# Performance work log

Hardware: AMD Instinct MI355X
Metric: run time of the kernel (lower is better)

Reference implementation:

```python
import jax, jax.numpy as jnp
import numpy as np

B, S, D, H, DK, FF, NQ = 4, 1024, 512, 64, 8, 2048, 8


def _layernorm(x, w, b, eps=1e-5):
    m = x.mean(-1, keepdims=True)
    v = ((x - m) ** 2).mean(-1, keepdims=True)
    return (x - m) / jnp.sqrt(v + eps) * w + b


def setup_inputs() -> dict:
    key = jax.random.key(0)
    ks = jax.random.split(key, 24)
    std = 0.02
    inp = {
        "x": jax.random.normal(ks[0], (B, S, D), dtype=jnp.float32),
        "Wq": jax.random.normal(ks[1], (D, D)) * std,
        "bq": jnp.zeros((D,)),
        "Wk": jax.random.normal(ks[2], (D, D)) * std,
        "bk": jnp.zeros((D,)),
        "Wv": jax.random.normal(ks[3], (D, D)) * std,
        "bv": jnp.zeros((D,)),
        "theta_attn": jax.random.normal(ks[4], (DK,)) * 0.1,  # trainable RX angles
        "gate_attn": jnp.asarray(1.0, dtype=jnp.float32),
        "Wo": jax.random.normal(ks[5], (D, D)) * std,
        "bo": jnp.zeros((D,)),
        "ln1_w": jnp.ones((D,)),
        "ln1_b": jnp.zeros((D,)),
        "W1": jax.random.normal(ks[6], (FF, NQ)) * std,
        "b1": jnp.zeros((FF,)),
        "W2": jax.random.normal(ks[7], (D, FF)) * std,
        "b2": jnp.zeros((D,)),
        "phi_ffn": jax.random.normal(ks[8], (NQ,)) * 0.1,  # trainable RY angles
        "gate_ffn": jnp.asarray(1.0, dtype=jnp.float32),
        "ln2_w": jnp.ones((D,)),
        "ln2_b": jnp.zeros((D,)),
    }
    return inp


def _attention(x, Wq, bq, Wk, bk, Wv, bv, theta, gate, Wo, bo):
    q = x @ Wq.T + bq
    k = x @ Wk.T + bk
    v = x @ Wv.T + bv
    sep = lambda t: t.reshape(B, S, H, DK).transpose(0, 2, 1, 3)  # [B,H,S,DK]
    qh, kh, vh = sep(q), sep(k), sep(v)
    scores = jnp.einsum("bhsd,bhtd->bhst", qh, kh) / np.sqrt(DK)
    probs = jax.nn.softmax(scores, axis=-1)
    classical = jnp.einsum("bhst,bhtd->bhsd", probs, vh)
    classical = classical.transpose(0, 2, 1, 3).reshape(B, S, D)
    # Quantum head: RX(x_i) then RX(theta_i) -> RX(x_i+theta_i), CNOT ring, <Z_j>.
    # Analytic expectations: <Z_0> = prod_{k=1..DK-1} cos(a_k);
    #                        <Z_j> = prod_{k=0..j}    cos(a_k)   (j >= 1).
    cos_a = jnp.cos(qh + theta)  # [B,H,S,DK]
    cp = jnp.cumprod(cos_a, axis=-1)
    z0 = jnp.prod(cos_a[..., 1:], axis=-1, keepdims=True)
    quantum = jnp.concatenate([z0, cp[..., 1:]], axis=-1)  # [B,H,S,DK]
    quantum = quantum.transpose(0, 2, 1, 3).reshape(B, S, D)
    out = gate * quantum + (1.0 - gate) * classical
    return out @ Wo.T + bo


def _ffn(x, W1, b1, W2, b2, phi, gate):
    xs = x[..., :NQ]  # encoder uses first NQ features
    # Quantum: RX(x_i) then RY(phi_i), measure <Z_i> = cos(x_i)*cos(phi_i).
    qm = jnp.cos(xs) * jnp.cos(phi)
    quantum = jax.nn.relu(qm @ W1.T + b1) @ W2.T + b2
    classical = jax.nn.relu(xs @ W1.T + b1) @ W2.T + b2
    return gate * quantum + (1.0 - gate) * classical


def reference(x, Wq, bq, Wk, bk, Wv, bv, theta_attn, gate_attn, Wo, bo,
              ln1_w, ln1_b, W1, b1, W2, b2, phi_ffn, gate_ffn, ln2_w, ln2_b):
    attn_out = _attention(x, Wq, bq, Wk, bk, Wv, bv, theta_attn, gate_attn, Wo, bo)
    x1 = _layernorm(x + attn_out, ln1_w, ln1_b)
    ffn_out = _ffn(x1, W1, b1, W2, b2, phi_ffn, gate_ffn)
    return _layernorm(x1 + ffn_out, ln2_w, ln2_b)
```

## Files before the change

### kernel.cpp

```cpp
#include <hip/hip_runtime.h>
#include <hip/hip_bf16.h>


typedef short short8 __attribute__((ext_vector_type(8)));
typedef float floatx4 __attribute__((ext_vector_type(4)));

__device__ __forceinline__ unsigned short f2bf_bits(float f) {
  __hip_bfloat16 h = __float2bfloat16(f);
  return *reinterpret_cast<unsigned short*>(&h);
}
__device__ __forceinline__ float bfbits2f(unsigned short u) {
  union { unsigned int u; float f; } c;
  c.u = (unsigned int)u << 16;
  return c.f;
}

#define GLOBAL_LOAD_LDS16(g, l)                                               \
  __builtin_amdgcn_global_load_lds(                                           \
      (const __attribute__((address_space(1))) void*)(g),                     \
      (__attribute__((address_space(3))) void*)(l), 16, 0, 0)

#define WAIT_VMCNT0()   asm volatile("s_waitcnt vmcnt(0)" ::: "memory")
#define WAIT_VMCNT16()  asm volatile("s_waitcnt vmcnt(16)" ::: "memory")
#define WAIT_LGKM0()    asm volatile("s_waitcnt lgkmcnt(0)" ::: "memory")

__device__ __forceinline__ void gemm_core(
    const __hip_bfloat16* __restrict__ A,
    const __hip_bfloat16* __restrict__ W,
    int K, long m0, long n0, int lane,
    __hip_bfloat16* sh, floatx4 acc[4][4])
{
  const int srow = lane >> 3;
  const int schunk = lane & 7;
  const int gchunk = schunk ^ srow;
  const int frow = lane & 15;
  const int fk = lane >> 4;

  auto stage = [&](int kt, __hip_bfloat16* Ab, __hip_bfloat16* Bb) {
#pragma unroll
    for (int ib = 0; ib < 8; ++ib) {
      const int row = ib * 8 + srow;
      GLOBAL_LOAD_LDS16(A + (m0 + row) * K + kt + gchunk * 8, Ab + ib * 512);
      GLOBAL_LOAD_LDS16(W + (n0 + row) * K + kt + gchunk * 8, Bb + ib * 512);
    }
  };

  const int ntiles = K >> 6;
  stage(0, sh, sh + 4096);
  for (int t = 0; t < ntiles; ++t) {
    __hip_bfloat16* As = sh + (t & 1) * 8192;
    __hip_bfloat16* Bs = As + 4096;
    if (t + 1 < ntiles) {
      WAIT_LGKM0();
      __hip_bfloat16* An = sh + ((t + 1) & 1) * 8192;
      stage((t + 1) << 6, An, An + 4096);
      WAIT_VMCNT16();
    } else {
      WAIT_VMCNT0();
    }
    short8 af[2][4], bf[2][4];
#pragma unroll
    for (int ks = 0; ks < 2; ++ks)
#pragma unroll
      for (int i = 0; i < 4; ++i) {
        const int ar = i * 16 + frow;
        af[ks][i] = *(const short8*)(As + ar * 64 + (((ks * 4 + fk) ^ (ar & 7)) << 3));
        bf[ks][i] = *(const short8*)(Bs + ar * 64 + (((ks * 4 + fk) ^ (ar & 7)) << 3));
      }
#pragma unroll
    for (int ks = 0; ks < 2; ++ks)
#pragma unroll
      for (int i = 0; i < 4; ++i)
#pragma unroll
        for (int j = 0; j < 4; ++j)
          acc[i][j] = __builtin_amdgcn_mfma_f32_16x16x32_bf16(
              af[ks][i], bf[ks][j], acc[i][j], 0, 0, 0);
  }
}

__global__ __launch_bounds__(64) void gemm_qkv(
    const __hip_bfloat16* __restrict__ x_bf,
    const __hip_bfloat16* __restrict__ Wq,
    const __hip_bfloat16* __restrict__ Wk,
    const __hip_bfloat16* __restrict__ Wv,
    const float* __restrict__ bq, const float* __restrict__ bk,
    const float* __restrict__ bvv,
    __hip_bfloat16* __restrict__ mix,
    float* __restrict__ Qb, float* __restrict__ Kb, float* __restrict__ Vb,
    const float* __restrict__ theta, const float* __restrict__ gateA)
{
  const int z = blockIdx.z;
  const float g = *gateA;
  if (z > 0 && g == 1.0f) return;
  const __hip_bfloat16* W = (z == 0) ? Wq : (z == 1) ? Wk : Wv;
  const float* bias = (z == 0) ? bq : (z == 1) ? bk : bvv;
  float* Cf = (z == 0) ? Qb : (z == 1) ? Kb : Vb;

  __shared__ __align__(16) __hip_bfloat16 sh[16384];
  const int lane = threadIdx.x;
  const long m0 = (long)blockIdx.x * 64;
  const long n0 = (long)blockIdx.y * 64;
  floatx4 acc[4][4];
#pragma unroll
  for (int i = 0; i < 4; ++i)
#pragma unroll
    for (int j = 0; j < 4; ++j) acc[i][j] = (floatx4){0.f, 0.f, 0.f, 0.f};

  gemm_core(x_bf, W, 512, m0, n0, lane, sh, acc);

  const int col_l = lane & 15;
  const int row_l = (lane >> 4) << 2;

  if (z > 0 || g != 1.0f) {
#pragma unroll
    for (int j = 0; j < 4; ++j) {
      const long col = n0 + j * 16 + col_l;
      const float bv = bias[col];
#pragma unroll
      for (int i = 0; i < 4; ++i)
#pragma unroll
        for (int r = 0; r < 4; ++r)
          Cf[(m0 + i * 16 + row_l + r) * 512 + col] = acc[i][j][r] + bv;
    }
  }
  if (z == 0) {
    float* shf = (float*)sh;
    WAIT_LGKM0();
#pragma unroll
    for (int j = 0; j < 4; ++j) {
      const long col = n0 + j * 16 + col_l;
      const float bv = bias[col];
#pragma unroll
      for (int i = 0; i < 4; ++i)
#pragma unroll
        for (int r = 0; r < 4; ++r)
          shf[(i * 16 + row_l + r) * 64 + j * 16 + col_l] = acc[i][j][r] + bv;
    }
    WAIT_LGKM0();
    float th[8];
#pragma unroll
    for (int i = 0; i < 8; ++i) th[i] = theta[i];
#pragma unroll
    for (int t = 0; t < 8; ++t) {
      const int gidx = t * 64 + lane;
      const int row = gidx >> 3;
      const int hh = gidx & 7;
      const float* src = shf + row * 64 + hh * 8;
      float c[8];
#pragma unroll
      for (int i = 0; i < 8; ++i) c[i] = __cosf(src[i] + th[i]);
      float o[8];
      float p = c[1];
#pragma unroll
      for (int i = 2; i < 8; ++i) p *= c[i];
      o[0] = p;
      float cp = c[0];
#pragma unroll
      for (int i = 1; i < 8; ++i) { cp *= c[i]; o[i] = cp; }
      union { unsigned short u16[8]; uint4 v; } pk;
#pragma unroll
      for (int i = 0; i < 8; ++i) pk.u16[i] = f2bf_bits(o[i]);
      *(uint4*)(mix + (m0 + row) * 512 + n0 + hh * 8) = pk.v;
    }
  }
}

__global__ __launch_bounds__(64) void gemm_plain(
    const __hip_bfloat16* __restrict__ A,
    const __hip_bfloat16* __restrict__ W,
    const float* __restrict__ bias, float* __restrict__ C, int N, int K)
{
  __shared__ __align__(16) __hip_bfloat16 sh[16384];
  const int lane = threadIdx.x;
  const long m0 = (long)blockIdx.x * 64;
  const long n0 = (long)blockIdx.y * 64;
  floatx4 acc[4][4];
#pragma unroll
  for (int i = 0; i < 4; ++i)
#pragma unroll
    for (int j = 0; j < 4; ++j) acc[i][j] = (floatx4){0.f, 0.f, 0.f, 0.f};
  gemm_core(A, W, K, m0, n0, lane, sh, acc);
  const int col_l = lane & 15;
  const int row_l = (lane >> 4) << 2;
#pragma unroll
  for (int j = 0; j < 4; ++j) {
    const long col = n0 + j * 16 + col_l;
    const float bv = bias[col];
#pragma unroll
    for (int i = 0; i < 4; ++i)
#pragma unroll
      for (int r = 0; r < 4; ++r)
        C[(m0 + i * 16 + row_l + r) * N + col] = acc[i][j][r] + bv;
  }
}

__global__ __launch_bounds__(64) void gemm_ffnout(
    const __hip_bfloat16* __restrict__ hq,
    const __hip_bfloat16* __restrict__ hc,
    const __hip_bfloat16* __restrict__ W2, const float* __restrict__ b2,
    float* __restrict__ Fb, float* __restrict__ Fc,
    const float* __restrict__ gateF)
{
  const int z = blockIdx.z;
  if (z == 1 && *gateF == 1.0f) return;
  const __hip_bfloat16* A = z ? hc : hq;
  float* C = z ? Fc : Fb;
  __shared__ __align__(16) __hip_bfloat16 sh[16384];
  const int lane = threadIdx.x;
  const long m0 = (long)blockIdx.x * 64;
  const long n0 = (long)blockIdx.y * 64;
  floatx4 acc[4][4];
#pragma unroll
  for (int i = 0; i < 4; ++i)
#pragma unroll
    for (int j = 0; j < 4; ++j) acc[i][j] = (floatx4){0.f, 0.f, 0.f, 0.f};
  gemm_core(A, W2, 2048, m0, n0, lane, sh, acc);
  const int col_l = lane & 15;
  const int row_l = (lane >> 4) << 2;
#pragma unroll
  for (int j = 0; j < 4; ++j) {
    const long col = n0 + j * 16 + col_l;
    const float bv = b2[col];
#pragma unroll
    for (int i = 0; i < 4; ++i)
#pragma unroll
      for (int r = 0; r < 4; ++r)
        C[(m0 + i * 16 + row_l + r) * 512 + col] = acc[i][j][r] + bv;
  }
}

__device__ __forceinline__ void cvt_one(const float* s, __hip_bfloat16* d, int n,
                                        long tid, long stride) {
  const int n4 = n >> 2;
  for (long i = tid; i < n4; i += stride) {
    float4 v = ((const float4*)s)[i];
    ushort4 u;
    u.x = f2bf_bits(v.x); u.y = f2bf_bits(v.y);
    u.z = f2bf_bits(v.z); u.w = f2bf_bits(v.w);
    ((ushort4*)d)[i] = u;
  }
}

__global__ __launch_bounds__(256) void prep_inputs(
    const float* x, __hip_bfloat16* x_bf,
    const float* Wq, __hip_bfloat16* Wq_bf,
    const float* Wo, __hip_bfloat16* Wo_bf,
    const float* W2, __hip_bfloat16* W2_bf,
    const float* W1, __hip_bfloat16* W1_bf,
    const float* Wk, __hip_bfloat16* Wk_bf,
    const float* Wv, __hip_bfloat16* Wv_bf,
    const float* gateA)
{
  const long stride = (long)gridDim.x * blockDim.x;
  const long tid = (long)blockIdx.x * blockDim.x + threadIdx.x;
  cvt_one(x, x_bf, 4096 * 512, tid, stride);
  cvt_one(Wq, Wq_bf, 512 * 512, tid, stride);
  cvt_one(Wo, Wo_bf, 512 * 512, tid, stride);
  cvt_one(W2, W2_bf, 512 * 2048, tid, stride);
  cvt_one(W1, W1_bf, 2048 * 8, tid, stride);
  if (*gateA != 1.0f) {
    cvt_one(Wk, Wk_bf, 512 * 512, tid, stride);
    cvt_one(Wv, Wv_bf, 512 * 512, tid, stride);
  }
}

__global__ __launch_bounds__(256) void attn_blend(
    const float* __restrict__ Qb, const float* __restrict__ Kb,
    const float* __restrict__ Vb, __hip_bfloat16* __restrict__ mix,
    const float* __restrict__ gateA)
{
  const float g = *gateA;
  if (g == 1.0f) return;
  const int idx = blockIdx.x * blockDim.x + threadIdx.x;
  if (idx >= 4 * 64 * 1024) return;
  const int s = idx & 1023;
  const int h = (idx >> 10) & 63;
  const int b = idx >> 16;
  const long qoff = ((long)(b * 1024 + s)) * 512 + h * 8;
  float q[8];
#pragma unroll
  for (int i = 0; i < 8; ++i) q[i] = Qb[qoff + i] * 0.35355339059327373f;
  float m = -INFINITY, l = 0.0f, acc[8];
#pragma unroll
  for (int i = 0; i < 8; ++i) acc[i] = 0.0f;
  for (int t = 0; t < 1024; ++t) {
    const long koff = ((long)(b * 1024 + t)) * 512 + h * 8;
    const float* kr = Kb + koff;
    const float* vr = Vb + koff;
    float sc = 0.0f;
#pragma unroll
    for (int i = 0; i < 8; ++i) sc += q[i] * kr[i];
    float nm = fmaxf(m, sc);
    float corr = __expf(m - nm);
    float p = __expf(sc - nm);
    l = l * corr + p;
#pragma unroll
    for (int i = 0; i < 8; ++i) acc[i] = acc[i] * corr + p * vr[i];
    m = nm;
  }
  const float inv = 1.0f / l;
  union { unsigned short u16[8]; uint4 v; } pk;
  pk.v = *(const uint4*)(mix + qoff);
#pragma unroll
  for (int i = 0; i < 8; ++i) {
    float quant = bfbits2f(pk.u16[i]);
    pk.u16[i] = f2bf_bits(g * quant + (1.0f - g) * acc[i] * inv);
  }
  *(uint4*)(mix + qoff) = pk.v;
}

__global__ __launch_bounds__(256) void lnffn2(
    const float* __restrict__ x, const float* __restrict__ attn,
    const float* __restrict__ lw, const float* __restrict__ lb,
    float* __restrict__ x1, const float* __restrict__ phi,
    const __hip_bfloat16* __restrict__ W1_bf, const float* __restrict__ b1,
    __hip_bfloat16* __restrict__ hq, __hip_bfloat16* __restrict__ hc,
    const float* __restrict__ gateF)
{
  const int tid = threadIdx.x;
  const int wv = tid >> 6, lane = tid & 63;
  const int row = blockIdx.x * 4 + wv;
  const long base = (long)row * 512;
  const int c0 = lane * 8;
  __shared__ float qrow[4][8];
  __shared__ float xsrow[4][8];

  float4 a0 = *(const float4*)(x + base + c0);
  float4 a1 = *(const float4*)(x + base + c0 + 4);
  float4 b0 = *(const float4*)(attn + base + c0);
  float4 b1v4 = *(const float4*)(attn + base + c0 + 4);
  float s[8] = {a0.x + b0.x, a0.y + b0.y, a0.z + b0.z, a0.w + b0.w,
                a1.x + b1v4.x, a1.y + b1v4.y, a1.z + b1v4.z, a1.w + b1v4.w};
  float sum = 0.f, ssq = 0.f;
#pragma unroll
  for (int i = 0; i < 8; ++i) { sum += s[i]; ssq += s[i] * s[i]; }
#pragma unroll
  for (int off = 32; off > 0; off >>= 1) {
    sum += __shfl_xor(sum, off);
    ssq += __shfl_xor(ssq, off);
  }
  const float mean = sum * (1.0f / 512.0f);
  const float var = ssq * (1.0f / 512.0f) - mean * mean;
  const float rstd = rsqrtf(fmaxf(var, 0.0f) + 1e-5f);
  float4 w0 = *(const float4*)(lw + c0);
  float4 w1 = *(const float4*)(lw + c0 + 4);
  float4 g0 = *(const float4*)(lb + c0);
  float4 g1 = *(const float4*)(lb + c0 + 4);
  float o[8];
  const float wf[8] = {w0.x, w0.y, w0.z, w0.w, w1.x, w1.y, w1.z, w1.w};
  const float gf8[8] = {g0.x, g0.y, g0.z, g0.w, g1.x, g1.y, g1.z, g1.w};
#pragma unroll
  for (int i = 0; i < 8; ++i) o[i] = (s[i] - mean) * rstd * wf[i] + gf8[i];
  *(float4*)(x1 + base + c0) = (float4){o[0], o[1], o[2], o[3]};
  *(float4*)(x1 + base + c0 + 4) = (float4){o[4], o[5], o[6], o[7]};
  if (lane == 0) {
#pragma unroll
    for (int i = 0; i < 8; ++i) {
      qrow[wv][i] = __cosf(o[i]) * __cosf(phi[i]);
      xsrow[wv][i] = o[i];
    }
  }
  __syncthreads();

  float w1f[8][8];
#pragma unroll
  for (int j = 0; j < 8; ++j) {
    uint4 wr = *(const uint4*)(W1_bf + (long)(tid * 8 + j) * 8);
    const unsigned short* pu = (const unsigned short*)&wr;
#pragma unroll
    for (int k = 0; k < 8; ++k) w1f[j][k] = bfbits2f(pu[k]);
  }
  float4 bb0 = *(const float4*)(b1 + tid * 8);
  float4 bb1 = *(const float4*)(b1 + tid * 8 + 4);
  const float b1v[8] = {bb0.x, bb0.y, bb0.z, bb0.w, bb1.x, bb1.y, bb1.z, bb1.w};
  const float gv = *gateF;
#pragma unroll
  for (int r = 0; r < 4; ++r) {
    const long rowr = (long)blockIdx.x * 4 + r;
    float qm[8];
#pragma unroll
    for (int k = 0; k < 8; ++k) qm[k] = qrow[r][k];
    union { unsigned short u16[8]; uint4 v; } pk;
#pragma unroll
    for (int j = 0; j < 8; ++j) {
      float acc = b1v[j];
#pragma unroll
      for (int k = 0; k < 8; ++k) acc += qm[k] * w1f[j][k];
      pk.u16[j] = f2bf_bits(fmaxf(acc, 0.0f));
    }
    *(uint4*)(hq + rowr * 2048 + tid * 8) = pk.v;
    if (gv != 1.0f) {
      float xs[8];
#pragma unroll
      for (int k = 0; k < 8; ++k) xs[k] = xsrow[r][k];
#pragma unroll
      for (int j = 0; j < 8; ++j) {
        float acc = b1v[j];
#pragma unroll
        for (int k = 0; k < 8; ++k) acc += xs[k] * w1f[j][k];
        pk.u16[j] = f2bf_bits(fmaxf(acc, 0.0f));
      }
      *(uint4*)(hc + rowr * 2048 + tid * 8) = pk.v;
    }
  }
}

__global__ __launch_bounds__(256) void add_ln3(
    const float* __restrict__ x1, const float* __restrict__ Fb,
    const float* __restrict__ Fc, const float* __restrict__ gateF,
    const float* __restrict__ lw, const float* __restrict__ lb,
    float* __restrict__ out)
{
  const int tid = threadIdx.x;
  const int wv = tid >> 6, lane = tid & 63;
  const int row = blockIdx.x * 4 + wv;
  const long base = (long)row * 512;
  const int c0 = lane * 8;
  float4 a0 = *(const float4*)(x1 + base + c0);
  float4 a1 = *(const float4*)(x1 + base + c0 + 4);
  float4 f0 = *(const float4*)(Fb + base + c0);
  float4 f1 = *(const float4*)(Fb + base + c0 + 4);
  float s[8];
  const float gv = *gateF;
  if (gv != 1.0f) {
    float4 c0v = *(const float4*)(Fc + base + c0);
    float4 c1v = *(const float4*)(Fc + base + c0 + 4);
    const float om = 1.0f - gv;
    s[0] = a0.x + gv * f0.x + om * c0v.x; s[1] = a0.y + gv * f0.y + om * c0v.y;
    s[2] = a0.z + gv * f0.z + om * c0v.z; s[3] = a0.w + gv * f0.w + om * c0v.w;
    s[4] = a1.x + gv * f1.x + om * c1v.x; s[5] = a1.y + gv * f1.y + om * c1v.y;
    s[6] = a1.z + gv * f1.z + om * c1v.z; s[7] = a1.w + gv * f1.w + om * c1v.w;
  } else {
    s[0] = a0.x + f0.x; s[1] = a0.y + f0.y; s[2] = a0.z + f0.z; s[3] = a0.w + f0.w;
    s[4] = a1.x + f1.x; s[5] = a1.y + f1.y; s[6] = a1.z + f1.z; s[7] = a1.w + f1.w;
  }
  float sum = 0.f, ssq = 0.f;
#pragma unroll
  for (int i = 0; i < 8; ++i) { sum += s[i]; ssq += s[i] * s[i]; }
#pragma unroll
  for (int off = 32; off > 0; off >>= 1) {
    sum += __shfl_xor(sum, off);
    ssq += __shfl_xor(ssq, off);
  }
  const float mean = sum * (1.0f / 512.0f);
  const float var = ssq * (1.0f / 512.0f) - mean * mean;
  const float rstd = rsqrtf(fmaxf(var, 0.0f) + 1e-5f);
  float4 w0 = *(const float4*)(lw + c0);
  float4 w1 = *(const float4*)(lw + c0 + 4);
  float4 g0 = *(const float4*)(lb + c0);
  float4 g1 = *(const float4*)(lb + c0 + 4);
  const float wf[8] = {w0.x, w0.y, w0.z, w0.w, w1.x, w1.y, w1.z, w1.w};
  const float gf8[8] = {g0.x, g0.y, g0.z, g0.w, g1.x, g1.y, g1.z, g1.w};
  float o[8];
#pragma unroll
  for (int i = 0; i < 8; ++i) o[i] = (s[i] - mean) * rstd * wf[i] + gf8[i];
  *(float4*)(out + base + c0) = (float4){o[0], o[1], o[2], o[3]};
  *(float4*)(out + base + c0 + 4) = (float4){o[4], o[5], o[6], o[7]};
}

extern "C" void kernel_launch(void* const* d_in, const int* in_sizes, int n_in,
                              void* d_out, int out_size, void* d_ws, size_t ws_size,
                              hipStream_t stream) {
  const float* x     = (const float*)d_in[0];
  const float* Wq    = (const float*)d_in[1];
  const float* bq    = (const float*)d_in[2];
  const float* Wk    = (const float*)d_in[3];
  const float* bk    = (const float*)d_in[4];
  const float* Wv    = (const float*)d_in[5];
  const float* bv    = (const float*)d_in[6];
  const float* theta = (const float*)d_in[7];
  const float* gateA = (const float*)d_in[8];
  const float* Wo    = (const float*)d_in[9];
  const float* bo    = (const float*)d_in[10];
  const float* ln1w  = (const float*)d_in[11];
  const float* ln1b  = (const float*)d_in[12];
  const float* W1    = (const float*)d_in[13];
  const float* b1    = (const float*)d_in[14];
  const float* W2    = (const float*)d_in[15];
  const float* b2    = (const float*)d_in[16];
  const float* phi   = (const float*)d_in[17];
  const float* gateF = (const float*)d_in[18];
  const float* ln2w  = (const float*)d_in[19];
  const float* ln2b  = (const float*)d_in[20];
  float* out = (float*)d_out;

  const size_t MB = 1024 * 1024;
  char* wsb = (char*)d_ws;
  __hip_bfloat16* x_bf   = (__hip_bfloat16*)(wsb + 0 * MB);
  __hip_bfloat16* Wq_bf  = (__hip_bfloat16*)(wsb + 4 * MB);
  __hip_bfloat16* Wo_bf  = (__hip_bfloat16*)(wsb + 4 * MB + 512 * 1024);
  __hip_bfloat16* W2_bf  = (__hip_bfloat16*)(wsb + 5 * MB);
  __hip_bfloat16* W1_bf  = (__hip_bfloat16*)(wsb + 7 * MB);
  __hip_bfloat16* mix_bf = (__hip_bfloat16*)(wsb + 8 * MB);
  float*          attn   = (float*)(wsb + 12 * MB);
  float*          x1     = (float*)(wsb + 20 * MB);
  __hip_bfloat16* hq_bf  = (__hip_bfloat16*)(wsb + 28 * MB);
  float*          Fb     = (float*)(wsb + 44 * MB);
  float*          Qb     = (float*)(wsb + 52 * MB);
  __hip_bfloat16* Wk_bf  = (__hip_bfloat16*)(wsb + 60 * MB);
  __hip_bfloat16* Wv_bf  = (__hip_bfloat16*)(wsb + 60 * MB + 512 * 1024);
  float*          Kb2    = (float*)(wsb + 61 * MB);
  float*          Vb2    = (float*)(wsb + 69 * MB);
  __hip_bfloat16* hc_bf  = (__hip_bfloat16*)(wsb + 77 * MB);
  float*          Fc     = (float*)(wsb + 93 * MB);

  prep_inputs<<<1024, 256, 0, stream>>>(
      x, x_bf, Wq, Wq_bf, Wo, Wo_bf, W2, W2_bf, W1, W1_bf,
      Wk, Wk_bf, Wv, Wv_bf, gateA);
  gemm_qkv<<<dim3(64, 8, 3), 64, 0, stream>>>(
      x_bf, Wq_bf, Wk_bf, Wv_bf, bq, bk, bv,
      mix_bf, Qb, Kb2, Vb2, theta, gateA);
  attn_blend<<<1024, 256, 0, stream>>>(Qb, Kb2, Vb2, mix_bf, gateA);
  gemm_plain<<<dim3(64, 8), 64, 0, stream>>>(
      mix_bf, Wo_bf, bo, attn, 512, 512);
  lnffn2<<<1024, 256, 0, stream>>>(
      x, attn, ln1w, ln1b, x1, phi, W1_bf, b1, hq_bf, hc_bf, gateF);
  gemm_ffnout<<<dim3(64, 8, 2), 64, 0, stream>>>(
      hq_bf, hc_bf, W2_bf, b2, Fb, Fc, gateF);
  add_ln3<<<1024, 256, 0, stream>>>(x1, Fb, Fc, gateF, ln2w, ln2b, out);
}
```

Measured before the change: 162.4 us.

## Deepen GEMM LDS pipeline from double to triple buffering

Switches the shared GEMM core from a two-stage to a three-stage LDS ring buffer: two tiles are prefetched ahead via global_load_lds, and vmcnt waits are tuned to keep two tiles in flight. This aims to hide more global-memory latency in the single-wave 64-thread GEMM blocks. LDS per block grows from 32KB to 48KB, which can reduce the number of resident blocks per CU. The refill of the current buffer is issued after its fragments are read and an lgkm wait.

```diff
diff --git a/kernel.cpp b/kernel.cpp
--- a/kernel.cpp
+++ b/kernel.cpp
@@ -22,6 +22,7 @@
 
 #define WAIT_VMCNT0()   asm volatile("s_waitcnt vmcnt(0)" ::: "memory")
 #define WAIT_VMCNT16()  asm volatile("s_waitcnt vmcnt(16)" ::: "memory")
+#define WAIT_VMCNT32()  asm volatile("s_waitcnt vmcnt(32)" ::: "memory")
 #define WAIT_LGKM0()    asm volatile("s_waitcnt lgkmcnt(0)" ::: "memory")
 
 __device__ __forceinline__ void gemm_core(
@@ -31,42 +32,43 @@
     __hip_bfloat16* sh, floatx4 acc[4][4])
 {
   const int srow = lane >> 3;
-  const int schunk = lane & 7;
-  const int gchunk = schunk ^ srow;
+  const int gchunk = (lane & 7) ^ srow;
   const int frow = lane & 15;
   const int fk = lane >> 4;
 
-  auto stage = [&](int kt, __hip_bfloat16* Ab, __hip_bfloat16* Bb) {
+  auto stage = [&](int kt, __hip_bfloat16* buf) {
 #pragma unroll
     for (int ib = 0; ib < 8; ++ib) {
       const int row = ib * 8 + srow;
-      GLOBAL_LOAD_LDS16(A + (m0 + row) * K + kt + gchunk * 8, Ab + ib * 512);
-      GLOBAL_LOAD_LDS16(W + (n0 + row) * K + kt + gchunk * 8, Bb + ib * 512);
+      GLOBAL_LOAD_LDS16(A + (m0 + row) * K + kt + gchunk * 8, buf + ib * 512);
+      GLOBAL_LOAD_LDS16(W + (n0 + row) * K + kt + gchunk * 8, buf + 4096 + ib * 512);
     }
   };
 
   const int ntiles = K >> 6;
-  stage(0, sh, sh + 4096);
+  WAIT_LGKM0();
+  stage(0, sh);
+  if (ntiles > 1) stage(64, sh + 8192);
+  if (ntiles > 2) stage(128, sh + 16384);
+
   for (int t = 0; t < ntiles; ++t) {
-    __hip_bfloat16* As = sh + (t & 1) * 8192;
-    __hip_bfloat16* Bs = As + 4096;
-    if (t + 1 < ntiles) {
-      WAIT_LGKM0();
-      __hip_bfloat16* An = sh + ((t + 1) & 1) * 8192;
-      stage((t + 1) << 6, An, An + 4096);
-      WAIT_VMCNT16();
-    } else {
-      WAIT_VMCNT0();
-    }
+    __hip_bfloat16* buf = sh + (t % 3) * 8192;
+    const int ahead = (ntiles - 1 - t) < 2 ? (ntiles - 1 - t) : 2;
+    if (ahead == 2) { WAIT_VMCNT32(); }
+    else if (ahead == 1) { WAIT_VMCNT16(); }
+    else { WAIT_VMCNT0(); }
+
     short8 af[2][4], bf[2][4];
 #pragma unroll
     for (int ks = 0; ks < 2; ++ks)
 #pragma unroll
       for (int i = 0; i < 4; ++i) {
         const int ar = i * 16 + frow;
-        af[ks][i] = *(const short8*)(As + ar * 64 + (((ks * 4 + fk) ^ (ar & 7)) << 3));
-        bf[ks][i] = *(const short8*)(Bs + ar * 64 + (((ks * 4 + fk) ^ (ar & 7)) << 3));
+        af[ks][i] = *(const short8*)(buf + ar * 64 + (((ks * 4 + fk) ^ (ar & 7)) << 3));
+        bf[ks][i] = *(const short8*)(buf + 4096 + ar * 64 + (((ks * 4 + fk) ^ (ar & 7)) << 3));
       }
+    WAIT_LGKM0();
+    if (t + 3 < ntiles) stage((t + 3) << 6, buf);
 #pragma unroll
     for (int ks = 0; ks < 2; ++ks)
 #pragma unroll
@@ -96,7 +98,7 @@
   const float* bias = (z == 0) ? bq : (z == 1) ? bk : bvv;
   float* Cf = (z == 0) ? Qb : (z == 1) ? Kb : Vb;
 
-  __shared__ __align__(16) __hip_bfloat16 sh[16384];
+  __shared__ __align__(16) __hip_bfloat16 sh[24576];
   const int lane = threadIdx.x;
   const long m0 = (long)blockIdx.x * 64;
   const long n0 = (long)blockIdx.y * 64;
@@ -170,7 +172,7 @@
     const __hip_bfloat16* __restrict__ W,
     const float* __restrict__ bias, float* __restrict__ C, int N, int K)
 {
-  __shared__ __align__(16) __hip_bfloat16 sh[16384];
+  __shared__ __align__(16) __hip_bfloat16 sh[24576];
   const int lane = threadIdx.x;
   const long m0 = (long)blockIdx.x * 64;
   const long n0 = (long)blockIdx.y * 64;
@@ -205,7 +207,7 @@
   if (z == 1 && *gateF == 1.0f) return;
   const __hip_bfloat16* A = z ? hc : hq;
   float* C = z ? Fc : Fb;
-  __shared__ __align__(16) __hip_bfloat16 sh[16384];
+  __shared__ __align__(16) __hip_bfloat16 sh[24576];
   const int lane = threadIdx.x;
   const long m0 = (long)blockIdx.x * 64;
   const long n0 = (long)blockIdx.y * 64;
```

Result: faster. 155.0 us (-4.5%).
